# Kernel tuning notes

Measured on AMD Instinct MI355X. Metric: run time of the kernel, lower is better.

The kernel has to match this reference:

```python
import jax, jax.numpy as jnp
import numpy as np

B = 16384
WIDE_DIM = 256          # 32 wide features * dim 8
DEEP_DIM = 1024         # 64 deep features * embedding_dim 16
SHARED = [2048, 1024, 512]
DOMAIN = [512, 256]
NUM_DOMAINS = 8


def setup_inputs() -> dict:
    key = jax.random.key(0)
    ks = jax.random.split(key, 20)
    s = 0.01  # embedding_init_var-style small init
    inp = {
        "wide_features": jax.random.normal(ks[0], (B, WIDE_DIM), jnp.float32),
        "deep_features": jax.random.normal(ks[1], (B, DEEP_DIM), jnp.float32),
        "domain_ids": jax.random.randint(ks[2], (B,), 0, NUM_DOMAINS, jnp.int64),
        # shared MLP (weights stored [in, out])
        "W1": jax.random.normal(ks[3], (DEEP_DIM, SHARED[0]), jnp.float32) * s,
        "b1": jnp.zeros((SHARED[0],), jnp.float32),
        "W2": jax.random.normal(ks[4], (SHARED[0], SHARED[1]), jnp.float32) * s,
        "b2": jnp.zeros((SHARED[1],), jnp.float32),
        "W3": jax.random.normal(ks[5], (SHARED[1], SHARED[2]), jnp.float32) * s,
        "b3": jnp.zeros((SHARED[2],), jnp.float32),
        # domain-specific MLP
        "Wd1": jax.random.normal(ks[6], (SHARED[2], DOMAIN[0]), jnp.float32) * s,
        "bd1": jnp.zeros((DOMAIN[0],), jnp.float32),
        "Wd2": jax.random.normal(ks[7], (DOMAIN[0], DOMAIN[1]), jnp.float32) * s,
        "bd2": jnp.zeros((DOMAIN[1],), jnp.float32),
        # per-domain output heads: Linear(DOMAIN[-1], 1) per domain
        "Wh": jax.random.normal(ks[8], (NUM_DOMAINS, DOMAIN[1]), jnp.float32) * s,
        "bh": jnp.zeros((NUM_DOMAINS,), jnp.float32),
    }
    return inp


def reference(wide_features, deep_features, domain_ids,
              W1, b1, W2, b2, W3, b3, Wd1, bd1, Wd2, bd2, Wh, bh):
    # wide part: sum embedding output to a scalar logit per sample [B, 1]
    wide = jnp.sum(wide_features, axis=1, keepdims=True)
    # shared deep MLP
    h = jax.nn.relu(deep_features @ W1 + b1)
    h = jax.nn.relu(h @ W2 + b2)
    shared = jax.nn.relu(h @ W3 + b3)          # [B, 512]
    # domain-specific tower (shared across domains)
    d = jax.nn.relu(shared @ Wd1 + bd1)
    d = jax.nn.relu(d @ Wd2 + bd2)             # [B, 256]
    # per-sample domain head routing: gather head weights, fused dot
    w = Wh[domain_ids]                          # [B, 256]
    head = jnp.sum(d * w, axis=1, keepdims=True) + bh[domain_ids][:, None]  # [B, 1]
    out = jax.nn.sigmoid(wide + head)
    return (out, shared, d)
```

## Files before the change

kernel.cpp:

```cpp
#include <hip/hip_runtime.h>
#include <hip/hip_bf16.h>


typedef __attribute__((ext_vector_type(8))) short short8;
typedef __attribute__((ext_vector_type(4))) float f32x4;

static __device__ __forceinline__ unsigned short f2bf_bits(float x) {
  __hip_bfloat16 h = __float2bfloat16(x);
  return __builtin_bit_cast(unsigned short, h);
}
static __device__ __forceinline__ float bf_bits2f(unsigned short u) {
  __hip_bfloat16 h = __builtin_bit_cast(__hip_bfloat16, u);
  return __bfloat162float(h);
}

static __device__ __forceinline__ void gload16(const void* g, void* l) {
  __builtin_amdgcn_global_load_lds(
      (const __attribute__((address_space(1))) void*)g,
      (__attribute__((address_space(3))) void*)l, 16, 0, 0);
}

static __device__ __forceinline__ unsigned lds_u32(const void* p) {
  return (unsigned)(uintptr_t)(const __attribute__((address_space(3))) void*)p;
}

static __device__ __forceinline__ short8 dsr(unsigned addr) {
  short8 r;
  asm volatile("ds_read_b128 %0, %1" : "=v"(r) : "v"(addr));
  return r;
}

#define MFMA16(a, b, c) __builtin_amdgcn_mfma_f32_16x16x32_bf16((a), (b), (c), 0, 0, 0)
#define SB0() __builtin_amdgcn_sched_barrier(0)
#define PRIO(x) __builtin_amdgcn_s_setprio(x)
#define BAR() __builtin_amdgcn_s_barrier()

__global__ void transpose_convert(const float* __restrict__ W,
                                  __hip_bfloat16* __restrict__ Wt,
                                  int K, int N) {
  __shared__ float tile[64][65];
  const int k0 = blockIdx.y * 64;
  const int n0 = blockIdx.x * 64;
  const int t  = threadIdx.x;
  const int tn = t & 63;
  const int t4 = t >> 6;
#pragma unroll
  for (int p = 0; p < 16; ++p) {
    int kl = p * 4 + t4;
    tile[kl][tn] = W[(size_t)(k0 + kl) * N + (n0 + tn)];
  }
  __syncthreads();
#pragma unroll
  for (int p = 0; p < 16; ++p) {
    int nl = p * 4 + t4;
    Wt[(size_t)(n0 + nl) * K + (k0 + tn)] = __float2bfloat16(tile[tn][nl]);
  }
}

__global__ void f32_to_bf16(const float* __restrict__ in,
                            unsigned short* __restrict__ out, int n8) {
  int i = blockIdx.x * blockDim.x + threadIdx.x;
  if (i >= n8) return;
  const f32x4* p = (const f32x4*)in + (size_t)i * 2;
  f32x4 a = p[0], b = p[1];
  short8 o;
  o[0] = (short)f2bf_bits(a[0]); o[1] = (short)f2bf_bits(a[1]);
  o[2] = (short)f2bf_bits(a[2]); o[3] = (short)f2bf_bits(a[3]);
  o[4] = (short)f2bf_bits(b[0]); o[5] = (short)f2bf_bits(b[1]);
  o[6] = (short)f2bf_bits(b[2]); o[7] = (short)f2bf_bits(b[3]);
  *(short8*)(out + (size_t)i * 8) = o;
}

__global__ __launch_bounds__(512, 2) void gemm_2b(
    const __hip_bfloat16* __restrict__ A,
    const __hip_bfloat16* __restrict__ Bt,
    const float* __restrict__ bias,
    __hip_bfloat16* __restrict__ Cb,
    float* __restrict__ Cf,
    int N, int K, int nbx) {
  __shared__ char lds[131072];

  const int tid  = threadIdx.x;
  const int lane = tid & 63;
  const int wid  = tid >> 6;
  const int wm   = wid >> 2;
  const int wn   = wid & 3;

  const int nwg = gridDim.x;
  const int cpx = nwg >> 3;
  const int id  = blockIdx.x;
  const int swz = (id & 7) * cpx + (id >> 3);
  const int bm  = (swz / nbx) * 256;
  const int bn  = (swz % nbx) * 256;

  const int ln15 = lane & 15;
  const unsigned cswz = (unsigned)((((lane >> 4) ^ (lane & 7)) << 4));

  const unsigned lbase = lds_u32(lds);
  const unsigned arow0 = lbase + (unsigned)(wm * 128 + ln15) * 128u + cswz;
  const unsigned brow0 = lbase + 32768u + (unsigned)(wn * 64 + ln15) * 128u + cswz;

  const int nt = K >> 6;

  const int swc = (tid & 7) ^ ((tid >> 3) & 7);
  const __hip_bfloat16* baseA = A  + (size_t)(bm + (tid >> 3)) * K + swc * 8;
  const __hip_bfloat16* baseB = Bt + (size_t)(bn + (tid >> 3)) * K + swc * 8;
  const unsigned ldst0 = (unsigned)(wid * 1024);

  auto stage = [&](int kt, int half, int isB) {
    const __hip_bfloat16* base = isB ? baseB : baseA;
    char* dst = lds + ((kt & 1) * 65536) + (isB ? 32768 : 0) + half * 16384;
#pragma unroll
    for (int q = 0; q < 2; ++q) {
      gload16(base + (size_t)((half * 128 + q * 64) * K + kt * 64),
              dst + q * 8192 + ldst0);
    }
  };

  f32x4 acc[8][4] = {};
  short8 aLo[4][2], aHi[4][2], b0v[2][2], b1v[2][2];

  stage(0, 0, 1); stage(0, 0, 0); stage(0, 1, 1); stage(0, 1, 0);
  if (nt > 1) {
    stage(1, 0, 1); stage(1, 0, 0);
    asm volatile("s_waitcnt vmcnt(4)");
  } else {
    asm volatile("s_waitcnt vmcnt(0)");
  }
  BAR();
#pragma unroll
  for (int mi = 0; mi < 4; ++mi) {
    unsigned ad = arow0 + (unsigned)(mi * 2048);
    aLo[mi][0] = dsr(ad); aLo[mi][1] = dsr(ad ^ 64u);
  }

  for (int t = 0; t < nt; ++t) {
    const unsigned po = (unsigned)(t & 1) * 65536u;
    const unsigned pn = po ^ 65536u;

    asm volatile("s_waitcnt lgkmcnt(0)");
    SB0();
#pragma unroll
    for (int nj = 0; nj < 2; ++nj) b0v[nj][0] = dsr(brow0 + po + (unsigned)(nj * 2048));
#pragma unroll
    for (int nj = 0; nj < 2; ++nj) b0v[nj][1] = dsr((brow0 + po + (unsigned)(nj * 2048)) ^ 64u);
#pragma unroll
    for (int nj = 0; nj < 2; ++nj) b1v[nj][0] = dsr(brow0 + po + (unsigned)((nj + 2) * 2048));
#pragma unroll
    for (int nj = 0; nj < 2; ++nj) b1v[nj][1] = dsr((brow0 + po + (unsigned)((nj + 2) * 2048)) ^ 64u);
    if (t + 1 < nt) stage(t + 1, 1, 1);
    asm volatile("s_waitcnt lgkmcnt(6)");
    SB0();
    PRIO(1);
#pragma unroll
    for (int mi = 0; mi < 4; ++mi)
#pragma unroll
      for (int nj = 0; nj < 2; ++nj)
        acc[mi][nj] = MFMA16(aLo[mi][0], b0v[nj][0], acc[mi][nj]);
    asm volatile("s_waitcnt lgkmcnt(4)");
    SB0();
#pragma unroll
    for (int mi = 0; mi < 4; ++mi)
#pragma unroll
      for (int nj = 0; nj < 2; ++nj)
        acc[mi][nj] = MFMA16(aLo[mi][1], b0v[nj][1], acc[mi][nj]);
    PRIO(0);

#pragma unroll
    for (int mi = 0; mi < 4; ++mi) {
      unsigned ad = arow0 + po + (unsigned)((mi + 4) * 2048);
      aHi[mi][0] = dsr(ad); aHi[mi][1] = dsr(ad ^ 64u);
    }
    if (t + 1 < nt) stage(t + 1, 1, 0);
    asm volatile("s_waitcnt lgkmcnt(8)");
    SB0();
    PRIO(1);
#pragma unroll
    for (int kk = 0; kk < 2; ++kk)
#pragma unroll
      for (int mi = 0; mi < 4; ++mi)
#pragma unroll
        for (int nj = 0; nj < 2; ++nj)
          acc[mi][nj + 2] = MFMA16(aLo[mi][kk], b1v[nj][kk], acc[mi][nj + 2]);
    PRIO(0);
    BAR();

    asm volatile("s_waitcnt lgkmcnt(0)");
    SB0();
    PRIO(1);
#pragma unroll
    for (int kk = 0; kk < 2; ++kk)
#pragma unroll
      for (int mi = 0; mi < 4; ++mi)
#pragma unroll
        for (int nj = 0; nj < 2; ++nj)
          acc[mi + 4][nj] = MFMA16(aHi[mi][kk], b0v[nj][kk], acc[mi + 4][nj]);
    PRIO(0);
    if (t + 2 < nt) stage(t + 2, 0, 1);
    if (t + 2 < nt)      asm volatile("s_waitcnt vmcnt(2)");
    else if (t + 1 < nt) asm volatile("s_waitcnt vmcnt(0)");
    if (t + 1 < nt) BAR();

    if (t + 1 < nt) {
#pragma unroll
      for (int mi = 0; mi < 4; ++mi) {
        unsigned ad = arow0 + pn + (unsigned)(mi * 2048);
        aLo[mi][0] = dsr(ad); aLo[mi][1] = dsr(ad ^ 64u);
      }
    }
    SB0();
    PRIO(1);
#pragma unroll
    for (int kk = 0; kk < 2; ++kk)
#pragma unroll
      for (int mi = 0; mi < 4; ++mi)
#pragma unroll
        for (int nj = 0; nj < 2; ++nj)
          acc[mi + 4][nj + 2] = MFMA16(aHi[mi][kk], b1v[nj][kk], acc[mi + 4][nj + 2]);
    PRIO(0);
    if (t + 2 < nt) stage(t + 2, 0, 0);
  }

  float biasv[4];
#pragma unroll
  for (int nj = 0; nj < 4; ++nj)
    biasv[nj] = bias[bn + wn * 64 + nj * 16 + ln15];

#pragma unroll
  for (int mi = 0; mi < 8; ++mi) {
    int row0 = bm + wm * 128 + mi * 16 + (lane >> 4) * 4;
#pragma unroll
    for (int nj = 0; nj < 4; ++nj) {
      int col = bn + wn * 64 + nj * 16 + ln15;
#pragma unroll
      for (int r = 0; r < 4; ++r) {
        float v = acc[mi][nj][r] + biasv[nj];
        v = v > 0.f ? v : 0.f;
        size_t idx = (size_t)(row0 + r) * N + col;
        Cb[idx] = __float2bfloat16(v);
        if (Cf) Cf[idx] = v;
      }
    }
  }
}

__global__ __launch_bounds__(512, 2) void gemm_128(
    const __hip_bfloat16* __restrict__ A,
    const __hip_bfloat16* __restrict__ Bt,
    const float* __restrict__ bias,
    __hip_bfloat16* __restrict__ Cb,
    float* __restrict__ Cf,
    int N, int K, int nbx) {
  __shared__ char lds[98304];

  const int tid  = threadIdx.x;
  const int lane = tid & 63;
  const int wid  = tid >> 6;
  const int wm   = wid >> 2;
  const int wn   = wid & 3;

  const int nwg = gridDim.x;
  const int cpx = nwg >> 3;
  const int id  = blockIdx.x;
  const int swz = (id & 7) * cpx + (id >> 3);
  const int bm  = (swz / nbx) * 128;
  const int bn  = (swz % nbx) * 256;

  const int ln15 = lane & 15;
  const unsigned cswz = (unsigned)((((lane >> 4) ^ (lane & 7)) << 4));

  const unsigned lbase = lds_u32(lds);
  const unsigned arow0 = lbase + (unsigned)(wm * 64 + ln15) * 128u + cswz;
  const unsigned brow0 = lbase + 16384u + (unsigned)(wn * 64 + ln15) * 128u + cswz;

  const int nt = K >> 6;

  const int swc = (tid & 7) ^ ((tid >> 3) & 7);
  const __hip_bfloat16* baseA = A  + (size_t)(bm + (tid >> 3)) * K + swc * 8;
  const __hip_bfloat16* baseB = Bt + (size_t)(bn + (tid >> 3)) * K + swc * 8;
  const unsigned ldst0 = (unsigned)(tid * 16);

  auto stageA = [&](int kt, int half) {
    char* dst = lds + ((kt & 1) * 49152) + half * 8192;
    gload16(baseA + (size_t)((half * 64) * K + kt * 64), dst + ldst0);
  };
  auto stageB = [&](int kt, int half) {
    char* dst = lds + ((kt & 1) * 49152) + 16384 + half * 16384;
#pragma unroll
    for (int q = 0; q < 2; ++q) {
      gload16(baseB + (size_t)((half * 128 + q * 64) * K + kt * 64),
              dst + q * 8192 + ldst0);
    }
  };

  f32x4 acc[4][4] = {};
  short8 aLo[2][2], aHi[2][2], b0v[2][2], b1v[2][2];

  stageB(0, 0); stageA(0, 0); stageB(0, 1); stageA(0, 1);
  if (nt > 1) {
    stageB(1, 0); stageA(1, 0);
    asm volatile("s_waitcnt vmcnt(3)");
  } else {
    asm volatile("s_waitcnt vmcnt(0)");
  }
  BAR();
#pragma unroll
  for (int mi = 0; mi < 2; ++mi) {
    unsigned ad = arow0 + (unsigned)(mi * 2048);
    aLo[mi][0] = dsr(ad); aLo[mi][1] = dsr(ad ^ 64u);
  }

  for (int t = 0; t < nt; ++t) {
    const unsigned po = (unsigned)(t & 1) * 49152u;
    const unsigned pn = po ^ 49152u;

    asm volatile("s_waitcnt lgkmcnt(0)");
    SB0();
#pragma unroll
    for (int nj = 0; nj < 2; ++nj) b0v[nj][0] = dsr(brow0 + po + (unsigned)(nj * 2048));
#pragma unroll
    for (int nj = 0; nj < 2; ++nj) b0v[nj][1] = dsr((brow0 + po + (unsigned)(nj * 2048)) ^ 64u);
#pragma unroll
    for (int nj = 0; nj < 2; ++nj) b1v[nj][0] = dsr(brow0 + po + (unsigned)((nj + 2) * 2048));
#pragma unroll
    for (int nj = 0; nj < 2; ++nj) b1v[nj][1] = dsr((brow0 + po + (unsigned)((nj + 2) * 2048)) ^ 64u);
    if (t + 1 < nt) stageB(t + 1, 1);
    asm volatile("s_waitcnt lgkmcnt(6)");
    SB0();
    PRIO(1);
#pragma unroll
    for (int mi = 0; mi < 2; ++mi)
#pragma unroll
      for (int nj = 0; nj < 2; ++nj)
        acc[mi][nj] = MFMA16(aLo[mi][0], b0v[nj][0], acc[mi][nj]);
    asm volatile("s_waitcnt lgkmcnt(4)");
    SB0();
#pragma unroll
    for (int mi = 0; mi < 2; ++mi)
#pragma unroll
      for (int nj = 0; nj < 2; ++nj)
        acc[mi][nj] = MFMA16(aLo[mi][1], b0v[nj][1], acc[mi][nj]);
    PRIO(0);

#pragma unroll
    for (int mi = 0; mi < 2; ++mi) {
      unsigned ad = arow0 + po + (unsigned)((mi + 2) * 2048);
      aHi[mi][0] = dsr(ad); aHi[mi][1] = dsr(ad ^ 64u);
    }
    if (t + 1 < nt) stageA(t + 1, 1);
    asm volatile("s_waitcnt lgkmcnt(4)");
    SB0();
    PRIO(1);
#pragma unroll
    for (int kk = 0; kk < 2; ++kk)
#pragma unroll
      for (int mi = 0; mi < 2; ++mi)
#pragma unroll
        for (int nj = 0; nj < 2; ++nj)
          acc[mi][nj + 2] = MFMA16(aLo[mi][kk], b1v[nj][kk], acc[mi][nj + 2]);
    PRIO(0);
    BAR();

    asm volatile("s_waitcnt lgkmcnt(0)");
    SB0();
    PRIO(1);
#pragma unroll
    for (int kk = 0; kk < 2; ++kk)
#pragma unroll
      for (int mi = 0; mi < 2; ++mi)
#pragma unroll
        for (int nj = 0; nj < 2; ++nj)
          acc[mi + 2][nj] = MFMA16(aHi[mi][kk], b0v[nj][kk], acc[mi + 2][nj]);
    PRIO(0);
    if (t + 2 < nt) stageB(t + 2, 0);
    if (t + 2 < nt)      asm volatile("s_waitcnt vmcnt(2)");
    else if (t + 1 < nt) asm volatile("s_waitcnt vmcnt(0)");
    if (t + 1 < nt) BAR();

    if (t + 1 < nt) {
#pragma unroll
      for (int mi = 0; mi < 2; ++mi) {
        unsigned ad = arow0 + pn + (unsigned)(mi * 2048);
        aLo[mi][0] = dsr(ad); aLo[mi][1] = dsr(ad ^ 64u);
      }
    }
    SB0();
    PRIO(1);
#pragma unroll
    for (int kk = 0; kk < 2; ++kk)
#pragma unroll
      for (int mi = 0; mi < 2; ++mi)
#pragma unroll
        for (int nj = 0; nj < 2; ++nj)
          acc[mi + 2][nj + 2] = MFMA16(aHi[mi][kk], b1v[nj][kk], acc[mi + 2][nj + 2]);
    PRIO(0);
    if (t + 2 < nt) stageA(t + 2, 0);
  }

  float biasv[4];
#pragma unroll
  for (int nj = 0; nj < 4; ++nj)
    biasv[nj] = bias[bn + wn * 64 + nj * 16 + ln15];

#pragma unroll
  for (int mi = 0; mi < 4; ++mi) {
    int row0 = bm + wm * 64 + mi * 16 + (lane >> 4) * 4;
#pragma unroll
    for (int nj = 0; nj < 4; ++nj) {
      int col = bn + wn * 64 + nj * 16 + ln15;
#pragma unroll
      for (int r = 0; r < 4; ++r) {
        float v = acc[mi][nj][r] + biasv[nj];
        v = v > 0.f ? v : 0.f;
        size_t idx = (size_t)(row0 + r) * N + col;
        Cb[idx] = __float2bfloat16(v);
        if (Cf) Cf[idx] = v;
      }
    }
  }
}

__global__ __launch_bounds__(256, 2) void gemm_bt(
    const __hip_bfloat16* __restrict__ A,
    const __hip_bfloat16* __restrict__ Bt,
    const float* __restrict__ bias,
    __hip_bfloat16* __restrict__ Cb,
    float* __restrict__ Cf,
    int N, int K) {
  __shared__ char lds[32768];

  const int tid  = threadIdx.x;
  const int lane = tid & 63;
  const int wid  = tid >> 6;
  const int wm   = wid >> 1;
  const int wn   = wid & 1;
  const int bm   = blockIdx.y * 128;
  const int bn   = blockIdx.x * 128;

  f32x4 acc[4][4] = {};

  const int srow = tid >> 3;
  const int sk   = (tid & 7) * 8;
  const int kTiles = K >> 6;

  for (int kt = 0; kt < kTiles; ++kt) {
    __syncthreads();
    const __hip_bfloat16* ga = A  + (size_t)(bm + srow) * K + kt * 64 + sk;
    const __hip_bfloat16* gb = Bt + (size_t)(bn + srow) * K + kt * 64 + sk;
#pragma unroll
    for (int p = 0; p < 4; ++p) {
      gload16(ga + (size_t)(p * 32) * K, &lds[p * 4096 + wid * 1024]);
      gload16(gb + (size_t)(p * 32) * K, &lds[16384 + p * 4096 + wid * 1024]);
    }
    __syncthreads();

#pragma unroll
    for (int kk = 0; kk < 2; ++kk) {
      short8 avec[4], bvec[4];
#pragma unroll
      for (int i = 0; i < 4; ++i) {
        int row = wm * 64 + i * 16 + (lane & 15);
        avec[i] = *(const short8*)&lds[row * 128 + kk * 64 + (lane >> 4) * 16];
      }
#pragma unroll
      for (int j = 0; j < 4; ++j) {
        int row = wn * 64 + j * 16 + (lane & 15);
        bvec[j] = *(const short8*)&lds[16384 + row * 128 + kk * 64 + (lane >> 4) * 16];
      }
#pragma unroll
      for (int i = 0; i < 4; ++i)
#pragma unroll
        for (int j = 0; j < 4; ++j)
          acc[i][j] = MFMA16(avec[i], bvec[j], acc[i][j]);
    }
  }

  float biasv[4];
#pragma unroll
  for (int j = 0; j < 4; ++j)
    biasv[j] = bias[bn + wn * 64 + j * 16 + (lane & 15)];

#pragma unroll
  for (int i = 0; i < 4; ++i) {
    int row0 = bm + wm * 64 + i * 16 + (lane >> 4) * 4;
#pragma unroll
    for (int j = 0; j < 4; ++j) {
      int col = bn + wn * 64 + j * 16 + (lane & 15);
#pragma unroll
      for (int r = 0; r < 4; ++r) {
        float v = acc[i][j][r] + biasv[j];
        v = v > 0.f ? v : 0.f;
        size_t idx = (size_t)(row0 + r) * N + col;
        Cb[idx] = __float2bfloat16(v);
        if (Cf) Cf[idx] = v;
      }
    }
  }
}

__global__ __launch_bounds__(256) void head_kernel(
    const float* __restrict__ wide,
    const __hip_bfloat16* __restrict__ D,
    const int* __restrict__ dom,
    const float* __restrict__ Wh,
    const float* __restrict__ bh,
    float* __restrict__ out, int B) {
  const int wid  = threadIdx.x >> 6;
  const int lane = threadIdx.x & 63;
  const int row  = blockIdx.x * 4 + wid;
  if (row >= B) return;
  const int dm = dom[row];

  f32x4 wv = ((const f32x4*)(wide + (size_t)row * 256))[lane];
  float tot = wv[0] + wv[1] + wv[2] + wv[3];

  const unsigned short* drow = (const unsigned short*)(D + (size_t)row * 256);
  ushort4 dv = ((const ushort4*)drow)[lane];
  f32x4 hv = ((const f32x4*)(Wh + (size_t)dm * 256))[lane];
  tot += bf_bits2f(dv.x) * hv[0] + bf_bits2f(dv.y) * hv[1] +
         bf_bits2f(dv.z) * hv[2] + bf_bits2f(dv.w) * hv[3];

#pragma unroll
  for (int off = 32; off > 0; off >>= 1) tot += __shfl_xor(tot, off);

  if (lane == 0) {
    float x = tot + bh[dm];
    out[row] = 1.f / (1.f + __expf(-x));
  }
}

extern "C" void kernel_launch(void* const* d_in, const int* in_sizes, int n_in,
                              void* d_out, int out_size, void* d_ws, size_t ws_size,
                              hipStream_t stream) {
  const float* wide = (const float*)d_in[0];
  const float* deep = (const float*)d_in[1];
  const int*   dom  = (const int*)d_in[2];
  const float* W1  = (const float*)d_in[3];
  const float* b1  = (const float*)d_in[4];
  const float* W2  = (const float*)d_in[5];
  const float* b2  = (const float*)d_in[6];
  const float* W3  = (const float*)d_in[7];
  const float* b3  = (const float*)d_in[8];
  const float* Wd1 = (const float*)d_in[9];
  const float* bd1 = (const float*)d_in[10];
  const float* Wd2 = (const float*)d_in[11];
  const float* bd2 = (const float*)d_in[12];
  const float* Wh  = (const float*)d_in[13];
  const float* bh  = (const float*)d_in[14];
  float* out = (float*)d_out;

  const int B = 16384;
  char* ws = (char*)d_ws;
  __hip_bfloat16* buf0 = (__hip_bfloat16*)ws;
  __hip_bfloat16* buf1 = (__hip_bfloat16*)(ws + 33554432ull);
  __hip_bfloat16* W1t  = (__hip_bfloat16*)(ws + 100663296ull);
  __hip_bfloat16* W2t  = W1t + 2048 * 1024;
  __hip_bfloat16* W3t  = W2t + 1024 * 2048;
  __hip_bfloat16* Wd1t = W3t + 512 * 1024;
  __hip_bfloat16* Wd2t = Wd1t + 512 * 512;

  transpose_convert<<<dim3(2048 / 64, 1024 / 64), 256, 0, stream>>>(W1, W1t, 1024, 2048);
  transpose_convert<<<dim3(1024 / 64, 2048 / 64), 256, 0, stream>>>(W2, W2t, 2048, 1024);
  transpose_convert<<<dim3(512 / 64, 1024 / 64), 256, 0, stream>>>(W3, W3t, 1024, 512);
  transpose_convert<<<dim3(512 / 64, 512 / 64), 256, 0, stream>>>(Wd1, Wd1t, 512, 512);
  transpose_convert<<<dim3(256 / 64, 512 / 64), 256, 0, stream>>>(Wd2, Wd2t, 512, 256);

  {
    int n8 = B * 1024 / 8;
    f32_to_bf16<<<(n8 + 255) / 256, 256, 0, stream>>>(deep, (unsigned short*)buf0, n8);
  }

  float* shared_out = out + B;
  float* d_out_f    = out + B + (size_t)B * 512;

  gemm_2b<<<dim3((2048 / 256) * (B / 256)), 512, 0, stream>>>(
      buf0, W1t, b1, buf1, nullptr, 2048, 1024, 2048 / 256);
  gemm_2b<<<dim3((1024 / 256) * (B / 256)), 512, 0, stream>>>(
      buf1, W2t, b2, buf0, nullptr, 1024, 2048, 1024 / 256);
  gemm_128<<<dim3((B / 128) * (512 / 256)), 512, 0, stream>>>(
      buf0, W3t, b3, buf1, shared_out, 512, 1024, 512 / 256);
  gemm_128<<<dim3((B / 128) * (512 / 256)), 512, 0, stream>>>(
      buf1, Wd1t, bd1, buf0, nullptr, 512, 512, 512 / 256);
  gemm_bt<<<dim3(256 / 128, B / 128), 256, 0, stream>>>(buf0, Wd2t, bd2, buf1, d_out_f, 256, 512);

  head_kernel<<<B / 4, 256, 0, stream>>>(wide, buf1, dom, Wh, bh, out, B);
}
```

Before: 224.4 us.

## Replace double-buffered gemm_2b with single-buffer templated GEMM allowing higher occupancy

Replaces the hand-scheduled double-buffered 256x256 GEMM with a templated single-buffered kernel (gemm_sb) that uses a smaller LDS footprint and declares launch bounds for four blocks per CU. The second GEMM now uses 256x128 tiles with 4 m-fragments per wave. The intent is to hide memory latency through more concurrent workgroups rather than explicit intra-block prefetch. In exchange, each k-step now waits on its full global load before computing, so load and compute no longer overlap within a block, and the register budget per thread is tighter.

```diff
diff --git a/kernel.cpp b/kernel.cpp
--- a/kernel.cpp
+++ b/kernel.cpp
@@ -71,154 +71,92 @@
   *(short8*)(out + (size_t)i * 8) = o;
 }
 
-__global__ __launch_bounds__(512, 2) void gemm_2b(
+template <int MI, int BN>
+__global__ __launch_bounds__(512, 4) void gemm_sb(
     const __hip_bfloat16* __restrict__ A,
     const __hip_bfloat16* __restrict__ Bt,
     const float* __restrict__ bias,
     __hip_bfloat16* __restrict__ Cb,
     float* __restrict__ Cf,
     int N, int K, int nbx) {
-  __shared__ char lds[131072];
+  constexpr int NWN = BN / 64;
+  __shared__ char lds[32768 + BN * 128];
 
   const int tid  = threadIdx.x;
   const int lane = tid & 63;
   const int wid  = tid >> 6;
-  const int wm   = wid >> 2;
-  const int wn   = wid & 3;
+  const int wm   = wid / NWN;
+  const int wn   = wid % NWN;
 
   const int nwg = gridDim.x;
   const int cpx = nwg >> 3;
   const int id  = blockIdx.x;
   const int swz = (id & 7) * cpx + (id >> 3);
   const int bm  = (swz / nbx) * 256;
-  const int bn  = (swz % nbx) * 256;
+  const int bn  = (swz % nbx) * BN;
 
   const int ln15 = lane & 15;
   const unsigned cswz = (unsigned)((((lane >> 4) ^ (lane & 7)) << 4));
-
   const unsigned lbase = lds_u32(lds);
-  const unsigned arow0 = lbase + (unsigned)(wm * 128 + ln15) * 128u + cswz;
-  const unsigned brow0 = lbase + 32768u + (unsigned)(wn * 64 + ln15) * 128u + cswz;
+  const unsigned aoff = lbase + (unsigned)((wm * (MI * 16) + ln15) * 128) + cswz;
+  const unsigned boff = lbase + 32768u + (unsigned)((wn * 64 + ln15) * 128) + cswz;
 
   const int nt = K >> 6;
-
   const int swc = (tid & 7) ^ ((tid >> 3) & 7);
   const __hip_bfloat16* baseA = A  + (size_t)(bm + (tid >> 3)) * K + swc * 8;
   const __hip_bfloat16* baseB = Bt + (size_t)(bn + (tid >> 3)) * K + swc * 8;
-  const unsigned ldst0 = (unsigned)(wid * 1024);
-
-  auto stage = [&](int kt, int half, int isB) {
-    const __hip_bfloat16* base = isB ? baseB : baseA;
-    char* dst = lds + ((kt & 1) * 65536) + (isB ? 32768 : 0) + half * 16384;
-#pragma unroll
-    for (int q = 0; q < 2; ++q) {
-      gload16(base + (size_t)((half * 128 + q * 64) * K + kt * 64),
-              dst + q * 8192 + ldst0);
-    }
+  const unsigned ldst0 = (unsigned)(tid * 16);
+
+  auto stage = [&](int kt) {
+#pragma unroll
+    for (int q = 0; q < 4; ++q)
+      gload16(baseA + (size_t)((q * 64) * K + kt * 64), lds + q * 8192 + ldst0);
+#pragma unroll
+    for (int q = 0; q < NWN; ++q)
+      gload16(baseB + (size_t)((q * 64) * K + kt * 64),
+              lds + 32768 + q * 8192 + ldst0);
   };
 
-  f32x4 acc[8][4] = {};
-  short8 aLo[4][2], aHi[4][2], b0v[2][2], b1v[2][2];
-
-  stage(0, 0, 1); stage(0, 0, 0); stage(0, 1, 1); stage(0, 1, 0);
-  if (nt > 1) {
-    stage(1, 0, 1); stage(1, 0, 0);
-    asm volatile("s_waitcnt vmcnt(4)");
-  } else {
+  f32x4 acc[MI][4] = {};
+
+  stage(0);
+  for (int t = 0; t < nt; ++t) {
     asm volatile("s_waitcnt vmcnt(0)");
-  }
-  BAR();
-#pragma unroll
-  for (int mi = 0; mi < 4; ++mi) {
-    unsigned ad = arow0 + (unsigned)(mi * 2048);
-    aLo[mi][0] = dsr(ad); aLo[mi][1] = dsr(ad ^ 64u);
-  }
-
-  for (int t = 0; t < nt; ++t) {
-    const unsigned po = (unsigned)(t & 1) * 65536u;
-    const unsigned pn = po ^ 65536u;
-
-    asm volatile("s_waitcnt lgkmcnt(0)");
-    SB0();
-#pragma unroll
-    for (int nj = 0; nj < 2; ++nj) b0v[nj][0] = dsr(brow0 + po + (unsigned)(nj * 2048));
-#pragma unroll
-    for (int nj = 0; nj < 2; ++nj) b0v[nj][1] = dsr((brow0 + po + (unsigned)(nj * 2048)) ^ 64u);
-#pragma unroll
-    for (int nj = 0; nj < 2; ++nj) b1v[nj][0] = dsr(brow0 + po + (unsigned)((nj + 2) * 2048));
-#pragma unroll
-    for (int nj = 0; nj < 2; ++nj) b1v[nj][1] = dsr((brow0 + po + (unsigned)((nj + 2) * 2048)) ^ 64u);
-    if (t + 1 < nt) stage(t + 1, 1, 1);
-    asm volatile("s_waitcnt lgkmcnt(6)");
-    SB0();
-    PRIO(1);
-#pragma unroll
-    for (int mi = 0; mi < 4; ++mi)
-#pragma unroll
-      for (int nj = 0; nj < 2; ++nj)
-        acc[mi][nj] = MFMA16(aLo[mi][0], b0v[nj][0], acc[mi][nj]);
-    asm volatile("s_waitcnt lgkmcnt(4)");
-    SB0();
-#pragma unroll
-    for (int mi = 0; mi < 4; ++mi)
-#pragma unroll
-      for (int nj = 0; nj < 2; ++nj)
-        acc[mi][nj] = MFMA16(aLo[mi][1], b0v[nj][1], acc[mi][nj]);
-    PRIO(0);
-
-#pragma unroll
-    for (int mi = 0; mi < 4; ++mi) {
-      unsigned ad = arow0 + po + (unsigned)((mi + 4) * 2048);
-      aHi[mi][0] = dsr(ad); aHi[mi][1] = dsr(ad ^ 64u);
-    }
-    if (t + 1 < nt) stage(t + 1, 1, 0);
-    asm volatile("s_waitcnt lgkmcnt(8)");
-    SB0();
-    PRIO(1);
-#pragma unroll
-    for (int kk = 0; kk < 2; ++kk)
-#pragma unroll
-      for (int mi = 0; mi < 4; ++mi)
-#pragma unroll
-        for (int nj = 0; nj < 2; ++nj)
-          acc[mi][nj + 2] = MFMA16(aLo[mi][kk], b1v[nj][kk], acc[mi][nj + 2]);
-    PRIO(0);
     BAR();
 
-    asm volatile("s_waitcnt lgkmcnt(0)");
-    SB0();
-    PRIO(1);
-#pragma unroll
-    for (int kk = 0; kk < 2; ++kk)
-#pragma unroll
-      for (int mi = 0; mi < 4; ++mi)
-#pragma unroll
-        for (int nj = 0; nj < 2; ++nj)
-          acc[mi + 4][nj] = MFMA16(aHi[mi][kk], b0v[nj][kk], acc[mi + 4][nj]);
-    PRIO(0);
-    if (t + 2 < nt) stage(t + 2, 0, 1);
-    if (t + 2 < nt)      asm volatile("s_waitcnt vmcnt(2)");
-    else if (t + 1 < nt) asm volatile("s_waitcnt vmcnt(0)");
-    if (t + 1 < nt) BAR();
-
-    if (t + 1 < nt) {
-#pragma unroll
-      for (int mi = 0; mi < 4; ++mi) {
-        unsigned ad = arow0 + pn + (unsigned)(mi * 2048);
-        aLo[mi][0] = dsr(ad); aLo[mi][1] = dsr(ad ^ 64u);
-      }
-    }
-    SB0();
-    PRIO(1);
-#pragma unroll
-    for (int kk = 0; kk < 2; ++kk)
-#pragma unroll
-      for (int mi = 0; mi < 4; ++mi)
-#pragma unroll
-        for (int nj = 0; nj < 2; ++nj)
-          acc[mi + 4][nj + 2] = MFMA16(aHi[mi][kk], b1v[nj][kk], acc[mi + 4][nj + 2]);
-    PRIO(0);
-    if (t + 2 < nt) stage(t + 2, 0, 0);
+    short8 bv[4][2];
+#pragma unroll
+    for (int nj = 0; nj < 4; ++nj)
+#pragma unroll
+      for (int kk = 0; kk < 2; ++kk)
+        bv[nj][kk] = dsr((boff + (unsigned)(nj * 2048)) ^ (unsigned)(kk << 6));
+    short8 aC[2], aN[2];
+    aC[0] = dsr(aoff);
+    aC[1] = dsr(aoff ^ 64u);
+
+#pragma unroll
+    for (int mi = 0; mi < MI; ++mi) {
+      if (mi + 1 < MI) {
+        unsigned ad = aoff + (unsigned)((mi + 1) * 2048);
+        aN[0] = dsr(ad);
+        aN[1] = dsr(ad ^ 64u);
+        asm volatile("s_waitcnt lgkmcnt(2)");
+      } else {
+        asm volatile("s_waitcnt lgkmcnt(0)");
+      }
+      SB0();
+      PRIO(1);
+#pragma unroll
+      for (int kk = 0; kk < 2; ++kk)
+#pragma unroll
+        for (int nj = 0; nj < 4; ++nj)
+          acc[mi][nj] = MFMA16(aC[kk], bv[nj][kk], acc[mi][nj]);
+      PRIO(0);
+      aC[0] = aN[0];
+      aC[1] = aN[1];
+    }
+    BAR();
+    if (t + 1 < nt) stage(t + 1);
   }
 
   float biasv[4];
@@ -227,8 +165,8 @@
     biasv[nj] = bias[bn + wn * 64 + nj * 16 + ln15];
 
 #pragma unroll
-  for (int mi = 0; mi < 8; ++mi) {
-    int row0 = bm + wm * 128 + mi * 16 + (lane >> 4) * 4;
+  for (int mi = 0; mi < MI; ++mi) {
+    int row0 = bm + wm * (MI * 16) + mi * 16 + (lane >> 4) * 4;
 #pragma unroll
     for (int nj = 0; nj < 4; ++nj) {
       int col = bn + wn * 64 + nj * 16 + ln15;
@@ -573,10 +511,10 @@
   float* shared_out = out + B;
   float* d_out_f    = out + B + (size_t)B * 512;
 
-  gemm_2b<<<dim3((2048 / 256) * (B / 256)), 512, 0, stream>>>(
+  gemm_sb<8, 256><<<dim3(512), 512, 0, stream>>>(
       buf0, W1t, b1, buf1, nullptr, 2048, 1024, 2048 / 256);
-  gemm_2b<<<dim3((1024 / 256) * (B / 256)), 512, 0, stream>>>(
-      buf1, W2t, b2, buf0, nullptr, 1024, 2048, 1024 / 256);
+  gemm_sb<4, 128><<<dim3(512), 512, 0, stream>>>(
+      buf1, W2t, b2, buf0, nullptr, 1024, 2048, 1024 / 128);
   gemm_128<<<dim3((B / 128) * (512 / 256)), 512, 0, stream>>>(
       buf0, W3t, b3, buf1, shared_out, 512, 1024, 512 / 256);
   gemm_128<<<dim3((B / 128) * (512 / 256)), 512, 0, stream>>>(
```

New measurement: 667.4 us. 197% more time.
